# Performance work log

Measured on AMD Instinct MI355X. Metric: run time of the kernel, lower is better.

Reference implementation:

```python
import jax, jax.numpy as jnp
import numpy as np
from jax import lax

N_HEADS = 8
KERNEL = 3
PAD = 1
D_MODEL = 512

def setup_inputs() -> dict:
    key = jax.random.key(0)
    k1, k2, k3 = jax.random.split(key, 3)
    x = jax.random.normal(k1, (64, 1024, D_MODEL), dtype=jnp.float32)
    weight = jax.random.normal(k2, (N_HEADS, 1, KERNEL), dtype=jnp.float32)
    fc_w = jax.random.normal(k3, (D_MODEL, D_MODEL), dtype=jnp.float32) * (1.0 / np.sqrt(D_MODEL))
    return {"x": x, "weight": weight, "fc_w": fc_w}

def reference(x, weight, fc_w):
    bs, gs, d_model = x.shape
    # weight_softmax=True: normalize kernel taps per head
    w = jax.nn.softmax(weight, axis=-1)  # [H, 1, K]
    # view(-1, n_heads, d_model): channels = heads, spatial axis = d_model
    x2 = x.reshape(-1, N_HEADS, d_model)  # [bs*gs/H, H, d_model]
    out = lax.conv_general_dilated(
        x2, w,
        window_strides=(1,),
        padding=[(PAD, PAD)],
        feature_group_count=N_HEADS,
        dimension_numbers=("NCH", "OIH", "NCH"),
    )  # depthwise conv along d_model
    out = out.reshape(bs, gs, d_model)
    # nn.Linear without bias: y = out @ fc_w.T
    return jnp.einsum("bgd,ed->bge", out, fc_w)
```

## Files before the change

### kernel.cpp

```cpp
#include <hip/hip_runtime.h>

typedef __attribute__((ext_vector_type(8))) __bf16  bf16x8;
typedef __attribute__((ext_vector_type(8))) short   short8;
typedef __attribute__((ext_vector_type(4))) float   f32x4;

#define DM   512
#define BM   256
#define BN   256
#define BK   64
#define NNT  2
#define NKT  8
#define TILEB 32768

__device__ __forceinline__ short f2bf(float f) {
  union { float f; unsigned u; } v; v.f = f;
  unsigned r = v.u + 0x7fffu + ((v.u >> 16) & 1u);
  return (short)(r >> 16);
}

__device__ __forceinline__ int swz(int r, int cbyte) {
  return (r * 128 + cbyte) ^ ((r & 7) << 4);
}

__global__ void build_g_kernel(const float* __restrict__ w,
                               const float* __restrict__ fcw,
                               short* __restrict__ Gt) {
  int idx = blockIdx.x * 256 + threadIdx.x;
  int h  = idx >> 15;
  int t  = idx & 32767;
  int e  = t >> 6;
  int d0 = (t & 63) << 3;
  float w0 = w[h*3+0], w1 = w[h*3+1], w2 = w[h*3+2];
  float mx = fmaxf(w0, fmaxf(w1, w2));
  float e0 = __expf(w0-mx), e1 = __expf(w1-mx), e2 = __expf(w2-mx);
  float inv = 1.0f / (e0 + e1 + e2);
  float w0n = e0*inv, w1n = e1*inv, w2n = e2*inv;
  const float* row = fcw + e * DM;
  float v[10];
  v[0] = (d0 > 0) ? row[d0-1] : 0.0f;
  float4 a = *(const float4*)(row + d0);
  float4 b = *(const float4*)(row + d0 + 4);
  v[1]=a.x; v[2]=a.y; v[3]=a.z; v[4]=a.w;
  v[5]=b.x; v[6]=b.y; v[7]=b.z; v[8]=b.w;
  v[9] = (d0 + 8 < DM) ? row[d0+8] : 0.0f;
  short8 sv;
  #pragma unroll
  for (int j = 0; j < 8; ++j)
    sv[j] = f2bf(w1n*v[j+1] + w0n*v[j+2] + w2n*v[j]);
  int nt = e >> 8, r = e & 255;
  int kt = d0 >> 6, c = d0 & 63;
  char* tile = (char*)Gt + (size_t)((h * NNT + nt) * NKT + kt) * TILEB;
  *(short8*)(tile + swz(r, c * 2)) = sv;
}

__global__ __launch_bounds__(512, 2) void gemm_kernel(const float* __restrict__ x,
                                                      const short* __restrict__ Gt,
                                                      float* __restrict__ out) {
  int bid = blockIdx.x;
  int h  = bid & 7;
  int nt = (bid >> 3) & 1;
  int mt = bid >> 4;
  int tid  = threadIdx.x;
  int lane = tid & 63;
  int wid  = tid >> 6;
  int wr = wid >> 2, wc = wid & 3;

  __shared__ short Alds[2][BM * BK];
  __shared__ short Blds[2][BN * BK];

  const char* Bsrc0 = (const char*)Gt + (size_t)(h * NNT + nt) * NKT * TILEB;
  const float* Abase = x + (size_t)(h + 8 * (size_t)mt * BM) * DM;

  float4 ap[8];

  auto loadA = [&](int kt) {
    #pragma unroll
    for (int p = 0; p < 4; ++p) {
      int r = (tid >> 3) + 64 * p;
      const float* xr = Abase + (size_t)r * 8 * DM + kt * BK + (tid & 7) * 8;
      ap[2*p]   = *(const float4*)xr;
      ap[2*p+1] = *(const float4*)(xr + 4);
    }
  };
  auto stageB = [&](int kt, int buf) {
    const char* src = Bsrc0 + kt * TILEB;
    char* dst = (char*)Blds[buf];
    #pragma unroll
    for (int p = 0; p < 4; ++p)
      __builtin_amdgcn_global_load_lds((const void*)(src + p * 8192 + tid * 16),
                                       (void*)(dst + p * 8192 + wid * 1024), 16, 0, 0);
  };
  auto writeA = [&](int buf) {
    char* dst = (char*)Alds[buf];
    #pragma unroll
    for (int p = 0; p < 4; ++p) {
      int r = (tid >> 3) + 64 * p;
      short8 sv;
      sv[0]=f2bf(ap[2*p].x);   sv[1]=f2bf(ap[2*p].y);
      sv[2]=f2bf(ap[2*p].z);   sv[3]=f2bf(ap[2*p].w);
      sv[4]=f2bf(ap[2*p+1].x); sv[5]=f2bf(ap[2*p+1].y);
      sv[6]=f2bf(ap[2*p+1].z); sv[7]=f2bf(ap[2*p+1].w);
      *(short8*)(dst + swz(r, (tid & 7) * 16)) = sv;
    }
  };

  f32x4 acc[8][4] = {};

  auto rdA = [&](bf16x8* af, const char* Ap, int mh, int ks) {
    #pragma unroll
    for (int m = 0; m < 4; ++m)
      af[m] = *(const bf16x8*)(Ap + swz(wr*128 + (mh*4 + m)*16 + (lane & 15),
                                        ks*64 + (lane >> 4) * 16));
  };
  auto rdB = [&](bf16x8* bfr, const char* Bp, int ks) {
    #pragma unroll
    for (int n = 0; n < 4; ++n)
      bfr[n] = *(const bf16x8*)(Bp + swz(wc*64 + n*16 + (lane & 15),
                                         ks*64 + (lane >> 4) * 16));
  };
  auto mma16 = [&](bf16x8* af, bf16x8* bfr, int mh) {
    #pragma unroll
    for (int m = 0; m < 4; ++m)
      #pragma unroll
      for (int n = 0; n < 4; ++n)
        acc[mh*4 + m][n] = __builtin_amdgcn_mfma_f32_16x16x32_bf16(af[m], bfr[n],
                                                                   acc[mh*4 + m][n], 0, 0, 0);
  };

#define SBAR()  do { __builtin_amdgcn_s_barrier(); __builtin_amdgcn_sched_barrier(0); } while (0)
#define LGKM0() do { asm volatile("s_waitcnt lgkmcnt(0)" ::: "memory"); \
                     __builtin_amdgcn_sched_barrier(0); } while (0)

  loadA(0);
  stageB(0, 0);
  writeA(0);
  __syncthreads();

  for (int kt = 0; kt < NKT; ++kt) {
    int nxt = (kt & 1) ^ 1;
    const char* Ap = (const char*)Alds[kt & 1];
    const char* Bp = (const char*)Blds[kt & 1];
    bool pre = (kt + 1 < NKT);
    bf16x8 af[4], bf0[4];

    rdB(bf0, Bp, 0); rdA(af, Ap, 0, 0);
    if (pre) loadA(kt + 1);
    SBAR(); LGKM0();
    __builtin_amdgcn_s_setprio(1); mma16(af, bf0, 0); __builtin_amdgcn_s_setprio(0);
    SBAR();

    rdA(af, Ap, 1, 0);
    if (pre) stageB(kt + 1, nxt);
    SBAR(); LGKM0();
    __builtin_amdgcn_s_setprio(1); mma16(af, bf0, 1); __builtin_amdgcn_s_setprio(0);
    SBAR();

    rdB(bf0, Bp, 1); rdA(af, Ap, 0, 1);
    SBAR(); LGKM0();
    __builtin_amdgcn_s_setprio(1); mma16(af, bf0, 0); __builtin_amdgcn_s_setprio(0);
    SBAR();

    rdA(af, Ap, 1, 1);
    SBAR(); LGKM0();
    __builtin_amdgcn_s_setprio(1); mma16(af, bf0, 1); __builtin_amdgcn_s_setprio(0);
    if (pre) writeA(nxt);
    __syncthreads();
  }

  int e0 = nt * BN + wc * 64 + (lane & 15);
  #pragma unroll
  for (int m = 0; m < 8; ++m) {
    int tq = mt * BM + wr * 128 + m * 16 + ((lane >> 4) << 2);
    #pragma unroll
    for (int j = 0; j < 4; ++j) {
      int R = h + 8 * (tq + j);
      float* orow = out + (size_t)R * DM + e0;
      #pragma unroll
      for (int n = 0; n < 4; ++n)
        orow[n * 16] = acc[m][n][j];
    }
  }
#undef SBAR
#undef LGKM0
}

extern "C" void kernel_launch(void* const* d_in, const int* in_sizes, int n_in,
                              void* d_out, int out_size, void* d_ws, size_t ws_size,
                              hipStream_t stream) {
  const float* x   = (const float*)d_in[0];
  const float* w   = (const float*)d_in[1];
  const float* fcw = (const float*)d_in[2];
  float* out = (float*)d_out;
  short* Gt  = (short*)d_ws;

  hipLaunchKernelGGL(build_g_kernel, dim3((8 * DM * DM / 8) / 256), dim3(256), 0, stream,
                     w, fcw, Gt);
  hipLaunchKernelGGL(gemm_kernel, dim3(8 * 32 * NNT), dim3(512), 0, stream,
                     x, Gt, out);
}
```

Baseline: 88.79 us.

## Shrink GEMM tiles and load A fragments straight from global into registers

Tiles shrink from 256x256 to 128x128 with 256-thread blocks, which quadruples the grid. The A operand no longer goes through LDS: each wave loads its fp32 rows of x directly into registers in MFMA fragment layout and converts them to bf16 in place. Only B is double-buffered in LDS. The explicit barrier/setprio schedule is dropped, reducing LDS traffic and synchronisation at the cost of more redundant global reads of x, less register-level reuse, and no software prefetch of A across k-steps.

```diff
diff --git a/kernel.cpp b/kernel.cpp
--- a/kernel.cpp
+++ b/kernel.cpp
@@ -5,12 +5,12 @@
 typedef __attribute__((ext_vector_type(4))) float   f32x4;
 
 #define DM   512
-#define BM   256
-#define BN   256
+#define BM   128
+#define BN   128
 #define BK   64
-#define NNT  2
+#define NNT  4
 #define NKT  8
-#define TILEB 32768
+#define TILEB (BN*BK*2)
 
 __device__ __forceinline__ short f2bf(float f) {
   union { float f; unsigned u; } v; v.f = f;
@@ -47,130 +47,104 @@
   #pragma unroll
   for (int j = 0; j < 8; ++j)
     sv[j] = f2bf(w1n*v[j+1] + w0n*v[j+2] + w2n*v[j]);
-  int nt = e >> 8, r = e & 255;
+  int nt = e >> 7, r = e & 127;
   int kt = d0 >> 6, c = d0 & 63;
   char* tile = (char*)Gt + (size_t)((h * NNT + nt) * NKT + kt) * TILEB;
   *(short8*)(tile + swz(r, c * 2)) = sv;
 }
 
-__global__ __launch_bounds__(512, 2) void gemm_kernel(const float* __restrict__ x,
+__global__ __launch_bounds__(256, 3) void gemm_kernel(const float* __restrict__ x,
                                                       const short* __restrict__ Gt,
                                                       float* __restrict__ out) {
   int bid = blockIdx.x;
-  int h  = bid & 7;
-  int nt = (bid >> 3) & 1;
-  int mt = bid >> 4;
+  int h   = bid & 7;
+  int idx = bid >> 3;
+  int nt  = idx & 3;
+  int mt  = idx >> 2;
   int tid  = threadIdx.x;
   int lane = tid & 63;
   int wid  = tid >> 6;
-  int wr = wid >> 2, wc = wid & 3;
+  int wr = wid >> 1, wc = wid & 1;
 
-  __shared__ short Alds[2][BM * BK];
   __shared__ short Blds[2][BN * BK];
 
   const char* Bsrc0 = (const char*)Gt + (size_t)(h * NNT + nt) * NKT * TILEB;
-  const float* Abase = x + (size_t)(h + 8 * (size_t)mt * BM) * DM;
+  const float* Arow0 = x + (size_t)(h + 8 * ((size_t)mt * BM + wr * 64 + (lane & 15))) * DM
+                         + (lane >> 4) * 8;
 
-  float4 ap[8];
-
-  auto loadA = [&](int kt) {
-    #pragma unroll
-    for (int p = 0; p < 4; ++p) {
-      int r = (tid >> 3) + 64 * p;
-      const float* xr = Abase + (size_t)r * 8 * DM + kt * BK + (tid & 7) * 8;
-      ap[2*p]   = *(const float4*)xr;
-      ap[2*p+1] = *(const float4*)(xr + 4);
-    }
-  };
   auto stageB = [&](int kt, int buf) {
     const char* src = Bsrc0 + kt * TILEB;
     char* dst = (char*)Blds[buf];
     #pragma unroll
     for (int p = 0; p < 4; ++p)
-      __builtin_amdgcn_global_load_lds((const void*)(src + p * 8192 + tid * 16),
-                                       (void*)(dst + p * 8192 + wid * 1024), 16, 0, 0);
+      __builtin_amdgcn_global_load_lds((const void*)(src + p * 4096 + tid * 16),
+                                       (void*)(dst + p * 4096 + wid * 1024), 16, 0, 0);
   };
-  auto writeA = [&](int buf) {
-    char* dst = (char*)Alds[buf];
+
+  f32x4 acc[4][4] = {};
+
+  auto loadAraw = [&](int kt, int ks, float4 (&raw)[8]) {
+    const float* base = Arow0 + kt * BK + ks * 32;
     #pragma unroll
-    for (int p = 0; p < 4; ++p) {
-      int r = (tid >> 3) + 64 * p;
-      short8 sv;
-      sv[0]=f2bf(ap[2*p].x);   sv[1]=f2bf(ap[2*p].y);
-      sv[2]=f2bf(ap[2*p].z);   sv[3]=f2bf(ap[2*p].w);
-      sv[4]=f2bf(ap[2*p+1].x); sv[5]=f2bf(ap[2*p+1].y);
-      sv[6]=f2bf(ap[2*p+1].z); sv[7]=f2bf(ap[2*p+1].w);
-      *(short8*)(dst + swz(r, (tid & 7) * 16)) = sv;
+    for (int m = 0; m < 4; ++m) {
+      const float* p = base + (size_t)(8 * 16 * m) * DM;
+      raw[2*m]   = *(const float4*)p;
+      raw[2*m+1] = *(const float4*)(p + 4);
     }
   };
-
-  f32x4 acc[8][4] = {};
-
-  auto rdA = [&](bf16x8* af, const char* Ap, int mh, int ks) {
+  auto cvtA = [&](const float4 (&raw)[8], bf16x8 (&af)[4]) {
     #pragma unroll
-    for (int m = 0; m < 4; ++m)
-      af[m] = *(const bf16x8*)(Ap + swz(wr*128 + (mh*4 + m)*16 + (lane & 15),
+    for (int m = 0; m < 4; ++m) {
+      bf16x8 v;
+      v[0]=(__bf16)raw[2*m].x;   v[1]=(__bf16)raw[2*m].y;
+      v[2]=(__bf16)raw[2*m].z;   v[3]=(__bf16)raw[2*m].w;
+      v[4]=(__bf16)raw[2*m+1].x; v[5]=(__bf16)raw[2*m+1].y;
+      v[6]=(__bf16)raw[2*m+1].z; v[7]=(__bf16)raw[2*m+1].w;
+      af[m] = v;
+    }
+  };
+  auto rdB = [&](const char* Bp, int ks, bf16x8 (&bf)[4]) {
+    #pragma unroll
+    for (int n = 0; n < 4; ++n)
+      bf[n] = *(const bf16x8*)(Bp + swz(wc*64 + n*16 + (lane & 15),
                                         ks*64 + (lane >> 4) * 16));
   };
-  auto rdB = [&](bf16x8* bfr, const char* Bp, int ks) {
-    #pragma unroll
-    for (int n = 0; n < 4; ++n)
-      bfr[n] = *(const bf16x8*)(Bp + swz(wc*64 + n*16 + (lane & 15),
-                                         ks*64 + (lane >> 4) * 16));
-  };
-  auto mma16 = [&](bf16x8* af, bf16x8* bfr, int mh) {
+  auto mma16 = [&](const bf16x8 (&af)[4], const bf16x8 (&bf)[4]) {
     #pragma unroll
     for (int m = 0; m < 4; ++m)
       #pragma unroll
       for (int n = 0; n < 4; ++n)
-        acc[mh*4 + m][n] = __builtin_amdgcn_mfma_f32_16x16x32_bf16(af[m], bfr[n],
-                                                                   acc[mh*4 + m][n], 0, 0, 0);
+        acc[m][n] = __builtin_amdgcn_mfma_f32_16x16x32_bf16(af[m], bf[n], acc[m][n], 0, 0, 0);
   };
 
-#define SBAR()  do { __builtin_amdgcn_s_barrier(); __builtin_amdgcn_sched_barrier(0); } while (0)
-#define LGKM0() do { asm volatile("s_waitcnt lgkmcnt(0)" ::: "memory"); \
-                     __builtin_amdgcn_sched_barrier(0); } while (0)
-
-  loadA(0);
   stageB(0, 0);
-  writeA(0);
   __syncthreads();
 
   for (int kt = 0; kt < NKT; ++kt) {
-    int nxt = (kt & 1) ^ 1;
-    const char* Ap = (const char*)Alds[kt & 1];
-    const char* Bp = (const char*)Blds[kt & 1];
-    bool pre = (kt + 1 < NKT);
-    bf16x8 af[4], bf0[4];
+    int cur = kt & 1;
+    const char* Bp = (const char*)Blds[cur];
+    float4 raw[8];
+    bf16x8 af[4], bf[4];
 
-    rdB(bf0, Bp, 0); rdA(af, Ap, 0, 0);
-    if (pre) loadA(kt + 1);
-    SBAR(); LGKM0();
-    __builtin_amdgcn_s_setprio(1); mma16(af, bf0, 0); __builtin_amdgcn_s_setprio(0);
-    SBAR();
+    loadAraw(kt, 0, raw);
+    if (kt + 1 < NKT) stageB(kt + 1, cur ^ 1);
 
-    rdA(af, Ap, 1, 0);
-    if (pre) stageB(kt + 1, nxt);
-    SBAR(); LGKM0();
-    __builtin_amdgcn_s_setprio(1); mma16(af, bf0, 1); __builtin_amdgcn_s_setprio(0);
-    SBAR();
+    cvtA(raw, af);
+    loadAraw(kt, 1, raw);
+    rdB(Bp, 0, bf);
+    mma16(af, bf);
 
-    rdB(bf0, Bp, 1); rdA(af, Ap, 0, 1);
-    SBAR(); LGKM0();
-    __builtin_amdgcn_s_setprio(1); mma16(af, bf0, 0); __builtin_amdgcn_s_setprio(0);
-    SBAR();
+    cvtA(raw, af);
+    rdB(Bp, 1, bf);
+    mma16(af, bf);
 
-    rdA(af, Ap, 1, 1);
-    SBAR(); LGKM0();
-    __builtin_amdgcn_s_setprio(1); mma16(af, bf0, 1); __builtin_amdgcn_s_setprio(0);
-    if (pre) writeA(nxt);
     __syncthreads();
   }
 
   int e0 = nt * BN + wc * 64 + (lane & 15);
   #pragma unroll
-  for (int m = 0; m < 8; ++m) {
-    int tq = mt * BM + wr * 128 + m * 16 + ((lane >> 4) << 2);
+  for (int m = 0; m < 4; ++m) {
+    int tq = mt * BM + wr * 64 + m * 16 + ((lane >> 4) << 2);
     #pragma unroll
     for (int j = 0; j < 4; ++j) {
       int R = h + 8 * (tq + j);
@@ -180,8 +154,6 @@
         orow[n * 16] = acc[m][n][j];
     }
   }
-#undef SBAR
-#undef LGKM0
 }
 
 extern "C" void kernel_launch(void* const* d_in, const int* in_sizes, int n_in,
@@ -195,6 +167,6 @@
 
   hipLaunchKernelGGL(build_g_kernel, dim3((8 * DM * DM / 8) / 256), dim3(256), 0, stream,
                      w, fcw, Gt);
-  hipLaunchKernelGGL(gemm_kernel, dim3(8 * 32 * NNT), dim3(512), 0, stream,
+  hipLaunchKernelGGL(gemm_kernel, dim3(8 * 64 * NNT), dim3(256), 0, stream,
                      x, Gt, out);
 }
```

After: 149.5 us. +68.4%, slower.
